# Optimization experiments

Hardware: AMD Instinct MI355X
Metric: run time of the kernel (lower is better)

The kernel has to match this reference:

```python
import jax, jax.numpy as jnp
import numpy as np

M, D, NI, L, NPL, R, T = 2, 128, 131072, 4, 2048, 8, 32
N = NI + L * NPL  # total DAG nodes


def setup_inputs() -> dict:
    key = jax.random.key(0)
    ks = jax.random.split(key, 18)
    thax = jax.random.randint(ks[0], (NI,), 0, T)
    sine = jax.random.uniform(ks[1], (NI,), jnp.float32)
    # parents of layer-l deriv nodes index any node built earlier (topological)
    raw = jax.random.randint(ks[2], (L, NPL, 2), 0, 2**30)
    bounds = jnp.array([NI + l * NPL for l in range(L)])[:, None, None]
    par = raw % bounds
    ridx = jax.random.randint(ks[3], (L, NPL), 0, R)
    pos = jax.random.uniform(ks[4], (N,), jnp.float32) + 0.01
    neg = jax.random.uniform(ks[5], (N,), jnp.float32) + 0.01
    s = 0.05
    return {
        'thax': thax, 'sine': sine, 'par': par, 'ridx': ridx,
        'pos': pos, 'neg': neg,
        'init_table': jax.random.normal(ks[6], (M, T, D)) * s,
        's_vec': jax.random.normal(ks[7], (M, D)) * s,
        'W1': jax.random.normal(ks[8], (M, R, 2 * D, D)) * s,
        'b1': jax.random.normal(ks[9], (M, R, D)) * s,
        'W2': jax.random.normal(ks[10], (M, R, D, D)) * s,
        'b2': jax.random.normal(ks[11], (M, R, D)) * s,
        'tweaks': jax.random.normal(ks[12], (M, 1, 2)) * s,
        'We1': jax.random.normal(ks[13], (M, D, D)) * s,
        'be1': jax.random.normal(ks[14], (M, D)) * s,
        'we2': jax.random.normal(ks[15], (M, D)) * s,
        'be2': jax.random.normal(ks[16], (M,)) * s,
    }


def reference(thax, sine, par, ridx, pos, neg, init_table, s_vec,
              W1, b1, W2, b2, tweaks, We1, be1, we2, be2):
    # init nodes: thax embedding + sine embellishment (per model)
    emb0 = init_table[:, thax, :] + sine[None, :, None] * s_vec[:, None, :]  # [M,NI,D]
    store = jnp.zeros((M, N, D), emb0.dtype).at[:, :NI].set(emb0)
    # topological layers of deriv nodes: gather parents, rule-indexed 2-layer MLP
    for l in range(L):
        p, r = par[l], ridx[l]
        cat = store[:, p].reshape(M, NPL, 2 * D)               # gather parents
        h = jax.nn.relu(jnp.einsum('mnc,mncd->mnd', cat, W1[:, r]) + b1[:, r])
        out = (jnp.einsum('mnd,mnde->mne', h, W2[:, r]) + b2[:, r]
               + tweaks[:, 0, 1][:, None, None])
        store = store.at[:, NI + l * NPL: NI + (l + 1) * NPL].set(out)
    # eval_net: per-node scalar logit (+ per-problem tweak)
    he = jax.nn.relu(jnp.einsum('mnd,mde->mne', store, We1) + be1[:, None, :])
    logit = jnp.einsum('mnd,md->mn', he, we2) + be2[:, None] + tweaks[:, 0, 0][:, None]
    tot_pos, tot_neg = pos.sum(), neg.sum()
    pw = tot_neg / tot_pos  # POS_WEIGHT_EXTRA = 1.0
    gold = pos / (pos + neg)
    w = pos + neg
    # BCEWithLogitsLoss(pos_weight=pw) per node, weighted by (pos+neg)
    bce = -(pw * gold[None] * jax.nn.log_sigmoid(logit)
            + (1.0 - gold[None]) * jax.nn.log_sigmoid(-logit))
    loss = (w[None] * bce).sum(axis=1)                          # [M]
    posOK = jnp.where(logit >= 0, pos[None], 0.0).sum(axis=1)
    negOK = jnp.where(logit < 0, neg[None], 0.0).sum(axis=1)
    return (loss, posOK, negOK, tot_pos, tot_neg)
```

## Files before the change

### kernel.cpp

```cpp
#include <hip/hip_runtime.h>
#include <hip/hip_bf16.h>

#define M_ 2
#define D_ 128
#define NI_ 131072
#define L_ 4
#define NPL_ 2048
#define R_ 8
#define T_ 32
#define N_ (NI_ + L_ * NPL_)
#define ND_ (L_ * NPL_)
#define PART3_ 1344

typedef __bf16 bf16x8 __attribute__((ext_vector_type(8)));
typedef float f32x4 __attribute__((ext_vector_type(4)));

#define OFF_W1T    0u
#define OFF_W2T    1048576u
#define OFF_WE1T   1572864u
#define OFF_TAB    1638400u
#define OFF_SVEC   1654784u
#define OFF_SORTED 1655296u
#define OFF_STARTS 1688064u
#define OFF_CNTF   1688192u
#define OFF_CNTA   1688320u
#define OFF_EA2    1688448u
#define OFF_EWB    1721216u
#define OFF_PA     1723264u
#define OFF_PB     1734016u
#define OFF_PPOK   1744768u
#define OFF_PNOK   1755520u
#define OFF_PTP    1766272u
#define OFF_PTN    1771648u
#define OFF_G      1777024u
#define OFF_STORE  2317696u
#define OFF_FSG    6512000u
#define OFF_CFG    6512032u
#define OFF_FLIST  6512064u

__device__ __forceinline__ unsigned short f2bu(float f) {
  unsigned int u = __float_as_uint(f);
  u += 0x7fffu + ((u >> 16) & 1u);
  return (unsigned short)(u >> 16);
}
__device__ __forceinline__ bf16x8 ldb8(const unsigned short* p) {
  return *reinterpret_cast<const bf16x8*>(p);
}

__device__ __forceinline__ bf16x8 node_chunk(int m, int row, int d0,
    const unsigned short* tab, const unsigned short* svec,
    const unsigned short* sd, const int* thax, const float* sine) {
  if (row < NI_) {
    bf16x8 tv = ldb8(&tab[(m * T_ + thax[row]) * D_ + d0]);
    bf16x8 sv = ldb8(&svec[m * D_ + d0]);
    float sn = sine[row];
    bf16x8 r;
#pragma unroll
    for (int j = 0; j < 8; ++j)
      r[j] = (__bf16)((float)tv[j] + sn * (float)sv[j]);
    return r;
  }
  return ldb8(&sd[(size_t)(m * ND_ + (row - NI_)) * D_ + d0]);
}

__global__ __launch_bounds__(256) void megaprep_kernel(
    const float* W1, const float* W2, const float* We1,
    const float* init_table, const float* s_vec,
    const float* b1, const float* be1, const float* we2,
    const int* ridx, const int* par,
    unsigned short* W1T, unsigned short* W2T, unsigned short* We1T,
    unsigned short* tab, unsigned short* svec,
    float* G, float* EA2, float* EWB,
    int* sorted, int* starts, int* cntF, int* cntA,
    int* fsg, int* cfg, int* fastlist, unsigned int* pzero) {
  __shared__ float smem[1056];
  __shared__ int icnt[16], ioff[16];
  int job = blockIdx.x;
  int tid = threadIdx.x;

  if (job < 800) {
    int z, rblk, cblk;
    if (job < 512)      { z = job >> 5;            rblk = (job & 31) >> 2; cblk = job & 3; }
    else if (job < 768) { int q = job - 512; z = 16 + (q >> 4); rblk = (q & 15) >> 2; cblk = q & 3; }
    else                { int q = job - 768; z = 32 + (q >> 4); rblk = (q & 15) >> 2; cblk = q & 3; }
    const float* src; unsigned short* dst; int R;
    if (z < 16)      { src = W1  + (size_t)z * 32768;        dst = W1T  + (size_t)z * 32768;        R = 256; }
    else if (z < 32) { src = W2  + (size_t)(z - 16) * 16384; dst = W2T  + (size_t)(z - 16) * 16384; R = 128; }
    else             { src = We1 + (size_t)(z - 32) * 16384; dst = We1T + (size_t)(z - 32) * 16384; R = 128; }
    int r0 = rblk * 32, c0 = cblk * 32;
    float (*tile)[33] = (float(*)[33])smem;
    int tx = tid & 31, ty = tid >> 5;
#pragma unroll
    for (int k = 0; k < 4; ++k)
      tile[ty + 8 * k][tx] = src[(size_t)(r0 + ty + 8 * k) * D_ + c0 + tx];
    __syncthreads();
#pragma unroll
    for (int k = 0; k < 4; ++k)
      dst[(size_t)(c0 + ty + 8 * k) * R + r0 + tx] = f2bu(tile[tx][ty + 8 * k]);
  } else if (job == 800) {
    for (int i = tid; i < 8448; i += 256) {
      if (i < 8192) tab[i] = f2bu(init_table[i]);
      else svec[i - 8192] = f2bu(s_vec[i - 8192]);
    }
  } else if (job < 1329) {
    int q = job - 801;
    int t = q / 16, mr = q & 15;
    int m = mr >> 3;
    int slot = tid >> 7, e = tid & 127;
    const float* vec = (t < 32) ? &init_table[(size_t)(m * T_ + t) * D_]
                                : &s_vec[(size_t)m * D_];
    if (tid < 128) smem[tid] = vec[tid];
    __syncthreads();
    const float* w = &W1[((size_t)mr * 256 + slot * 128) * D_];
    float acc = 0.f;
#pragma unroll 8
    for (int c = 0; c < 128; ++c) acc = fmaf(smem[c], w[c * D_ + e], acc);
    if (slot == 0 && t < 32) acc += b1[mr * D_ + e];
    G[((size_t)(mr * 2 + slot) * 33 + t) * D_ + e] = acc;
  } else if (job < 1363) {
    int q = job - 1329;
    int m = q / 17, t = (q % 17) * 2 + (tid >> 7);
    int e = tid & 127;
    if (t <= 32) {
      const float* vec = (t < 32) ? &init_table[(size_t)(m * T_ + t) * D_]
                                  : &s_vec[(size_t)m * D_];
      const float* w = &We1[(size_t)m * D_ * D_];
      float acc = 0.f;
#pragma unroll 8
      for (int d = 0; d < 128; ++d) acc = fmaf(vec[d], w[d * D_ + e], acc);
      if (t < 32) {
        EA2[m * 4096 + ((e >> 1) * 32 + t) * 2 + (e & 1)] = acc + be1[m * D_ + e];
      } else {
        EWB[(m * D_ + e) * 2 + 0] = acc;
        EWB[(m * D_ + e) * 2 + 1] = we2[m * D_ + e];
      }
    }
  } else if (job < 1367) {
    int l = job - 1363;
    if (tid < 16) icnt[tid] = 0;
    __syncthreads();
    for (int n = tid; n < NPL_; n += 256) {
      int r = ridx[l * NPL_ + n];
      int p0 = par[(l * NPL_ + n) * 2 + 0], p1 = par[(l * NPL_ + n) * 2 + 1];
      int slow = (p0 >= NI_ || p1 >= NI_) ? 1 : 0;
      atomicAdd(&icnt[r * 2 + slow], 1);
    }
    __syncthreads();
    if (tid == 0) {
      int run = 0;
      for (int b = 0; b < 16; ++b) { ioff[b] = run; run += icnt[b]; }
      for (int r = 0; r < R_; ++r) {
        starts[l * R_ + r] = ioff[2 * r];
        cntF[l * R_ + r] = icnt[2 * r];
        cntA[l * R_ + r] = icnt[2 * r] + icnt[2 * r + 1];
      }
    }
    __syncthreads();
    for (int n = tid; n < NPL_; n += 256) {
      int r = ridx[l * NPL_ + n];
      int p0 = par[(l * NPL_ + n) * 2 + 0], p1 = par[(l * NPL_ + n) * 2 + 1];
      int slow = (p0 >= NI_ || p1 >= NI_) ? 1 : 0;
      int p = atomicAdd(&ioff[r * 2 + slow], 1);
      sorted[l * NPL_ + p] = n;
    }
  } else if (job == 1367) {
    if (tid < 8) icnt[tid] = 0;
    __syncthreads();
    for (int g = tid; g < ND_; g += 256) {
      int p0 = par[2 * g], p1 = par[2 * g + 1];
      if (p0 < NI_ && p1 < NI_) atomicAdd(&icnt[ridx[g]], 1);
    }
    __syncthreads();
    if (tid == 0) {
      int run = 0;
      for (int r = 0; r < R_; ++r) {
        ioff[r] = run; fsg[r] = run; cfg[r] = icnt[r]; run += icnt[r];
      }
    }
    __syncthreads();
    for (int g = tid; g < ND_; g += 256) {
      int p0 = par[2 * g], p1 = par[2 * g + 1];
      if (p0 < NI_ && p1 < NI_) {
        int p = atomicAdd(&ioff[ridx[g]], 1);
        fastlist[p] = g;
      }
    }
  } else {
    for (int i = tid; i < 13440; i += 256) pzero[i] = 0u;
  }
}

__global__ __launch_bounds__(256) void main_kernel(
    const int* thax, const float* sine, const int* par,
    const float* pos, const float* neg,
    const float* b2, const float* tweaks,
    const float* G, const unsigned short* W2T, const unsigned short* We1T,
    const float* EA2, const float* EWB,
    const float* be1, const float* we2, const float* be2,
    const int* fsg, const int* cfg, const int* fastlist,
    unsigned short* sd,
    float* pA, float* pB, float* pPok, float* pNok, float* pTp, float* pTn) {
  __shared__ float sbuf[4448];
  int bid = blockIdx.x;
  int tid = threadIdx.x;
  int w = tid >> 6, lane = tid & 63;

  if (bid < 1280) {
    int m = bid / 640, q = bid % 640;
    int r = q / 80, tile = q % 80;
    int cnt = cfg[r];
    int base = tile * 16;
    if (base >= cnt) return;
    unsigned short* h_lds = (unsigned short*)sbuf;
    int*   t0a  = (int*)(sbuf + 1024);
    int*   t1a  = t0a + 16;
    float* s0a  = (float*)(t1a + 16);
    float* s1a  = s0a + 16;
    int*   gida = (int*)(s1a + 16);
    float* red2 = sbuf + 1104;
    if (tid < 16) {
      int loc = base + tid; if (loc >= cnt) loc = cnt - 1;
      int gid = fastlist[fsg[r] + loc];
      int p0 = par[2 * gid], p1 = par[2 * gid + 1];
      t0a[tid] = thax[p0]; s0a[tid] = sine[p0];
      t1a[tid] = thax[p1]; s1a[tid] = sine[p1];
      gida[tid] = gid;
    }
    __syncthreads();
    const float* Gm = &G[(size_t)(m * R_ + r) * 8448];
    {
      int row = tid >> 4, seg = tid & 15, d0 = seg * 8;
      int t0 = t0a[row], t1 = t1a[row];
      float s0 = s0a[row], s1 = s1a[row];
      const float* pa = &Gm[t0 * 128 + d0];
      const float* pb = &Gm[(33 + t1) * 128 + d0];
      const float* pu = &Gm[4096 + d0];
      const float* pv = &Gm[8320 + d0];
      bf16x8 hv;
#pragma unroll
      for (int half = 0; half < 2; ++half) {
        float4 a = *(const float4*)(pa + half * 4);
        float4 b = *(const float4*)(pb + half * 4);
        float4 u = *(const float4*)(pu + half * 4);
        float4 v = *(const float4*)(pv + half * 4);
        hv[half * 4 + 0] = (__bf16)fmaxf(a.x + b.x + s0 * u.x + s1 * v.x, 0.f);
        hv[half * 4 + 1] = (__bf16)fmaxf(a.y + b.y + s0 * u.y + s1 * v.y, 0.f);
        hv[half * 4 + 2] = (__bf16)fmaxf(a.z + b.z + s0 * u.z + s1 * v.z, 0.f);
        hv[half * 4 + 3] = (__bf16)fmaxf(a.w + b.w + s0 * u.w + s1 * v.w, 0.f);
      }
      *(bf16x8*)&h_lds[row * 128 + (d0 ^ ((row & 7) << 3))] = hv;
    }
    __syncthreads();
    int l15 = lane & 15, l4 = lane >> 4;
    const unsigned short* w2b = &W2T[(size_t)(m * R_ + r) * D_ * D_];
    f32x4 acc[2];
    acc[0] = (f32x4){0.f, 0.f, 0.f, 0.f};
    acc[1] = (f32x4){0.f, 0.f, 0.f, 0.f};
#pragma unroll
    for (int kc = 0; kc < 4; ++kc) {
      int d0 = kc * 32 + l4 * 8;
      bf16x8 a2 = ldb8(&h_lds[l15 * 128 + (d0 ^ ((l15 & 7) << 3))]);
#pragma unroll
      for (int f = 0; f < 2; ++f) {
        int fg = w * 2 + f;
        bf16x8 b = ldb8(&w2b[(fg * 16 + l15) * D_ + d0]);
        acc[f] = __builtin_amdgcn_mfma_f32_16x16x32_bf16(a2, b, acc[f], 0, 0, 0);
      }
    }
    float tw1 = tweaks[m * 2 + 1];
    const float* b2v = &b2[(m * R_ + r) * D_];
    __syncthreads();
#pragma unroll
    for (int i = 0; i < 4; ++i) {
      int row = l4 * 4 + i;
      int g = base + row;
#pragma unroll
      for (int f = 0; f < 2; ++f) {
        int e = (w * 2 + f) * 16 + l15;
        unsigned short val = f2bu(acc[f][i] + b2v[e] + tw1);
        h_lds[row * 128 + (e ^ ((row & 7) << 3))] = val;
        if (g < cnt) sd[(size_t)(m * ND_ + gida[row]) * D_ + e] = val;
      }
    }
    __syncthreads();
    f32x4 ae[2];
    ae[0] = (f32x4){0.f, 0.f, 0.f, 0.f};
    ae[1] = (f32x4){0.f, 0.f, 0.f, 0.f};
    const unsigned short* we1b = &We1T[(size_t)m * D_ * D_];
#pragma unroll
    for (int kc = 0; kc < 4; ++kc) {
      int d0 = kc * 32 + l4 * 8;
      bf16x8 a2 = ldb8(&h_lds[l15 * 128 + (d0 ^ ((l15 & 7) << 3))]);
#pragma unroll
      for (int f = 0; f < 2; ++f) {
        int fg = w * 2 + f;
        bf16x8 b = ldb8(&we1b[(fg * 16 + l15) * D_ + d0]);
        ae[f] = __builtin_amdgcn_mfma_f32_16x16x32_bf16(a2, b, ae[f], 0, 0, 0);
      }
    }
    float part[4] = {0.f, 0.f, 0.f, 0.f};
#pragma unroll
    for (int f = 0; f < 2; ++f) {
      int e = (w * 2 + f) * 16 + l15;
      float bb = be1[m * D_ + e];
      float wv = we2[m * D_ + e];
#pragma unroll
      for (int i = 0; i < 4; ++i) {
        float he = ae[f][i] + bb;
        he = he > 0.f ? he : 0.f;
        part[i] += he * wv;
      }
    }
#pragma unroll
    for (int mask = 1; mask < 16; mask <<= 1) {
#pragma unroll
      for (int i = 0; i < 4; ++i) part[i] += __shfl_xor(part[i], mask, 64);
    }
    if (l15 == 0) {
#pragma unroll
      for (int i = 0; i < 4; ++i) red2[w * 16 + l4 * 4 + i] = part[i];
    }
    __syncthreads();
    if (tid < 16) {
      int g = base + tid;
      float v6[6] = {0.f, 0.f, 0.f, 0.f, 0.f, 0.f};
      if (g < cnt) {
        float logit = red2[tid] + red2[16 + tid] + red2[32 + tid] + red2[48 + tid]
                    + be2[m] + tweaks[m * 2 + 0];
        int grow = NI_ + gida[tid];
        float p_ = pos[grow], n_ = neg[grow];
        float lse = log1pf(__expf(-fabsf(logit)));
        v6[0] = p_ * (fmaxf(-logit, 0.f) + lse);
        v6[1] = n_ * (fmaxf(logit, 0.f) + lse);
        v6[2] = logit >= 0.f ? p_ : 0.f;
        v6[3] = logit < 0.f ? n_ : 0.f;
        v6[4] = p_; v6[5] = n_;
      }
#pragma unroll
      for (int mask = 1; mask < 16; mask <<= 1) {
#pragma unroll
        for (int qq = 0; qq < 6; ++qq) v6[qq] += __shfl_xor(v6[qq], mask, 64);
      }
      if (tid == 0) {
        int slot = 512 + r * 80 + tile;
        pA[m * PART3_ + slot] = v6[0];
        pB[m * PART3_ + slot] = v6[1];
        pPok[m * PART3_ + slot] = v6[2];
        pNok[m * PART3_ + slot] = v6[3];
        if (m == 0) { pTp[slot] = v6[4]; pTn[slot] = v6[5]; }
      }
    }
  } else {
    int q = bid - 1280;
    int m = q >> 9, xb = q & 511;
    float* lea = sbuf;
    float* lwb = sbuf + 4096;
    float* red = sbuf + 4352;
    for (int i = tid; i < 4096; i += 256) lea[i] = EA2[m * 4096 + i];
    if (tid < 256) lwb[tid] = EWB[m * 256 + tid];
    __syncthreads();
    int row = xb * 256 + tid;
    int t = thax[row];
    float s = sine[row];
    float acc = 0.f;
#pragma unroll 8
    for (int p = 0; p < 64; ++p) {
      float2 ea = *(const float2*)&lea[(p * 32 + t) * 2];
      float4 wb = *(const float4*)&lwb[p * 4];
      float x0 = fmaf(s, wb.x, ea.x); x0 = fmaxf(x0, 0.f);
      acc = fmaf(x0, wb.y, acc);
      float x1 = fmaf(s, wb.z, ea.y); x1 = fmaxf(x1, 0.f);
      acc = fmaf(x1, wb.w, acc);
    }
    float logit = acc + be2[m] + tweaks[m * 2 + 0];
    float p_ = pos[row], n_ = neg[row];
    float lse = log1pf(__expf(-fabsf(logit)));
    float v[6];
    v[0] = p_ * (fmaxf(-logit, 0.f) + lse);
    v[1] = n_ * (fmaxf(logit, 0.f) + lse);
    v[2] = logit >= 0.f ? p_ : 0.f;
    v[3] = logit < 0.f ? n_ : 0.f;
    v[4] = p_; v[5] = n_;
#pragma unroll
    for (int mask = 1; mask < 64; mask <<= 1) {
#pragma unroll
      for (int k = 0; k < 6; ++k) v[k] += __shfl_xor(v[k], mask, 64);
    }
    if (lane == 0) {
#pragma unroll
      for (int k = 0; k < 6; ++k) red[k * 16 + w] = v[k];
    }
    __syncthreads();
    if (tid == 0) {
      float t6[6];
#pragma unroll
      for (int k = 0; k < 6; ++k)
        t6[k] = red[k * 16 + 0] + red[k * 16 + 1] + red[k * 16 + 2] + red[k * 16 + 3];
      pA[m * PART3_ + xb] = t6[0];
      pB[m * PART3_ + xb] = t6[1];
      pPok[m * PART3_ + xb] = t6[2];
      pNok[m * PART3_ + xb] = t6[3];
      if (m == 0) { pTp[xb] = t6[4]; pTn[xb] = t6[5]; }
    }
  }
}

__global__ __launch_bounds__(128) void slow_eval_kernel(int l,
    const int* thax, const float* sine, const int* par,
    const float* b1, const float* b2, const float* tweaks,
    const float* pos, const float* neg,
    const float* be1, const float* we2, const float* be2,
    const unsigned short* tab, const unsigned short* svec,
    const unsigned short* W1T, const unsigned short* W2T,
    const unsigned short* We1T,
    const int* sorted, const int* starts, const int* cntF, const int* cntA,
    unsigned short* sd,
    float* pA, float* pB, float* pPok, float* pNok, float* pTp, float* pTn) {
  int tile = blockIdx.x, r = blockIdx.y, m = blockIdx.z;
  int cF = cntF[l * R_ + r];
  int cS = cntA[l * R_ + r] - cF;
  int base = tile * 16;
  if (base >= cS) return;
  int start = starts[l * R_ + r] + cF;
  int tid = threadIdx.x;
  int w = tid >> 6, lane = tid & 63;
  int l15 = lane & 15, l4 = lane >> 4;
  __shared__ unsigned short h_lds[16 * 128];
  __shared__ float red2[32];

  int loc = base + l15; if (loc >= cS) loc = cS - 1;
  int node = sorted[l * NPL_ + start + loc];
  int p0 = par[(l * NPL_ + node) * 2 + 0];
  int p1 = par[(l * NPL_ + node) * 2 + 1];
  const unsigned short* w1b = &W1T[(size_t)(m * R_ + r) * D_ * 256];
  const unsigned short* w2b = &W2T[(size_t)(m * R_ + r) * D_ * D_];
  const unsigned short* we1b = &We1T[(size_t)m * D_ * D_];

  bf16x8 av[8];
#pragma unroll
  for (int kc = 0; kc < 8; ++kc) {
    int k = kc * 32 + l4 * 8;
    int p = (k < 128) ? p0 : p1;
    av[kc] = node_chunk(m, p, k & 127, tab, svec, sd, thax, sine);
  }
  f32x4 acch[4];
#pragma unroll
  for (int f = 0; f < 4; ++f) acch[f] = (f32x4){0.f, 0.f, 0.f, 0.f};
#pragma unroll
  for (int kc = 0; kc < 8; ++kc) {
    int k = kc * 32 + l4 * 8;
#pragma unroll
    for (int f = 0; f < 4; ++f) {
      int fg = w * 4 + f;
      bf16x8 b = ldb8(&w1b[(fg * 16 + l15) * 256 + k]);
      acch[f] = __builtin_amdgcn_mfma_f32_16x16x32_bf16(av[kc], b, acch[f], 0, 0, 0);
    }
  }
  const float* b1v = &b1[(m * R_ + r) * D_];
#pragma unroll
  for (int f = 0; f < 4; ++f) {
    int d = (w * 4 + f) * 16 + l15;
    float bb = b1v[d];
#pragma unroll
    for (int i = 0; i < 4; ++i) {
      int row = l4 * 4 + i;
      float h = acch[f][i] + bb;
      h = h > 0.f ? h : 0.f;
      h_lds[row * 128 + (d ^ ((row & 7) << 3))] = f2bu(h);
    }
  }
  __syncthreads();
  f32x4 acco[4];
#pragma unroll
  for (int f = 0; f < 4; ++f) acco[f] = (f32x4){0.f, 0.f, 0.f, 0.f};
#pragma unroll
  for (int kc = 0; kc < 4; ++kc) {
    int d0 = kc * 32 + l4 * 8;
    bf16x8 a2 = ldb8(&h_lds[l15 * 128 + (d0 ^ ((l15 & 7) << 3))]);
#pragma unroll
    for (int f = 0; f < 4; ++f) {
      int fg = w * 4 + f;
      bf16x8 b = ldb8(&w2b[(fg * 16 + l15) * D_ + d0]);
      acco[f] = __builtin_amdgcn_mfma_f32_16x16x32_bf16(a2, b, acco[f], 0, 0, 0);
    }
  }
  float tw1 = tweaks[m * 2 + 1];
  const float* b2v = &b2[(m * R_ + r) * D_];
  __syncthreads();
#pragma unroll
  for (int i = 0; i < 4; ++i) {
    int row = l4 * 4 + i;
    int g = base + row;
#pragma unroll
    for (int f = 0; f < 4; ++f) {
      int e = (w * 4 + f) * 16 + l15;
      unsigned short val = f2bu(acco[f][i] + b2v[e] + tw1);
      h_lds[row * 128 + (e ^ ((row & 7) << 3))] = val;
      if (g < cS) {
        int nd = sorted[l * NPL_ + start + g];
        sd[(size_t)(m * ND_ + l * NPL_ + nd) * D_ + e] = val;
      }
    }
  }
  __syncthreads();
  f32x4 ae[4];
#pragma unroll
  for (int f = 0; f < 4; ++f) ae[f] = (f32x4){0.f, 0.f, 0.f, 0.f};
#pragma unroll
  for (int kc = 0; kc < 4; ++kc) {
    int d0 = kc * 32 + l4 * 8;
    bf16x8 a2 = ldb8(&h_lds[l15 * 128 + (d0 ^ ((l15 & 7) << 3))]);
#pragma unroll
    for (int f = 0; f < 4; ++f) {
      int fg = w * 4 + f;
      bf16x8 b = ldb8(&we1b[(fg * 16 + l15) * D_ + d0]);
      ae[f] = __builtin_amdgcn_mfma_f32_16x16x32_bf16(a2, b, ae[f], 0, 0, 0);
    }
  }
  float part[4] = {0.f, 0.f, 0.f, 0.f};
#pragma unroll
  for (int f = 0; f < 4; ++f) {
    int e = (w * 4 + f) * 16 + l15;
    float bb = be1[m * D_ + e];
    float wv = we2[m * D_ + e];
#pragma unroll
    for (int i = 0; i < 4; ++i) {
      float he = ae[f][i] + bb;
      he = he > 0.f ? he : 0.f;
      part[i] += he * wv;
    }
  }
#pragma unroll
  for (int mask = 1; mask < 16; mask <<= 1) {
#pragma unroll
    for (int i = 0; i < 4; ++i) part[i] += __shfl_xor(part[i], mask, 64);
  }
  if (l15 == 0) {
#pragma unroll
    for (int i = 0; i < 4; ++i) red2[w * 16 + l4 * 4 + i] = part[i];
  }
  __syncthreads();
  if (tid < 16) {
    int g = base + tid;
    float v6[6] = {0.f, 0.f, 0.f, 0.f, 0.f, 0.f};
    if (g < cS) {
      float logit = red2[tid] + red2[16 + tid] + be2[m] + tweaks[m * 2 + 0];
      int nd = sorted[l * NPL_ + start + g];
      int grow = NI_ + l * NPL_ + nd;
      float p_ = pos[grow], n_ = neg[grow];
      float lse = log1pf(__expf(-fabsf(logit)));
      v6[0] = p_ * (fmaxf(-logit, 0.f) + lse);
      v6[1] = n_ * (fmaxf(logit, 0.f) + lse);
      v6[2] = logit >= 0.f ? p_ : 0.f;
      v6[3] = logit < 0.f ? n_ : 0.f;
      v6[4] = p_; v6[5] = n_;
    }
#pragma unroll
    for (int mask = 1; mask < 16; mask <<= 1) {
#pragma unroll
      for (int qq = 0; qq < 6; ++qq) v6[qq] += __shfl_xor(v6[qq], mask, 64);
    }
    if (tid == 0) {
      int slot = 1152 + (l - 1) * 64 + r * 8 + tile;
      pA[m * PART3_ + slot] = v6[0];
      pB[m * PART3_ + slot] = v6[1];
      pPok[m * PART3_ + slot] = v6[2];
      pNok[m * PART3_ + slot] = v6[3];
      if (m == 0) { pTp[slot] = v6[4]; pTn[slot] = v6[5]; }
    }
  }
}

__global__ __launch_bounds__(256) void finalize_kernel(
    const float* pA, const float* pB, const float* pPok, const float* pNok,
    const float* pTp, const float* pTn, float* out) {
  __shared__ float lred[10][4];
  const float* srcs[10] = {pA, pA + PART3_, pB, pB + PART3_,
                           pPok, pPok + PART3_, pNok, pNok + PART3_,
                           pTp, pTn};
  int tid = threadIdx.x;
  int w = tid >> 6, lane = tid & 63;
#pragma unroll
  for (int q = 0; q < 10; ++q) {
    float s = 0.f;
    for (int i = tid; i < PART3_; i += 256) s += srcs[q][i];
#pragma unroll
    for (int mask = 1; mask < 64; mask <<= 1) s += __shfl_xor(s, mask, 64);
    if (lane == 0) lred[q][w] = s;
  }
  __syncthreads();
  if (tid == 0) {
    float totals[10];
#pragma unroll
    for (int q = 0; q < 10; ++q)
      totals[q] = lred[q][0] + lred[q][1] + lred[q][2] + lred[q][3];
    float tp = totals[8], tn = totals[9];
    float pw = tn / tp;
    out[0] = pw * totals[0] + totals[2];
    out[1] = pw * totals[1] + totals[3];
    out[2] = totals[4]; out[3] = totals[5];
    out[4] = totals[6]; out[5] = totals[7];
    out[6] = tp; out[7] = tn;
  }
}

extern "C" void kernel_launch(void* const* d_in, const int* in_sizes, int n_in,
                              void* d_out, int out_size, void* d_ws, size_t ws_size,
                              hipStream_t stream) {
  const int*   thax = (const int*)d_in[0];
  const float* sine = (const float*)d_in[1];
  const int*   par  = (const int*)d_in[2];
  const int*   ridx = (const int*)d_in[3];
  const float* pos  = (const float*)d_in[4];
  const float* neg  = (const float*)d_in[5];
  const float* init_table = (const float*)d_in[6];
  const float* s_vec = (const float*)d_in[7];
  const float* W1 = (const float*)d_in[8];
  const float* b1 = (const float*)d_in[9];
  const float* W2 = (const float*)d_in[10];
  const float* b2 = (const float*)d_in[11];
  const float* tweaks = (const float*)d_in[12];
  const float* We1 = (const float*)d_in[13];
  const float* be1 = (const float*)d_in[14];
  const float* we2 = (const float*)d_in[15];
  const float* be2 = (const float*)d_in[16];

  char* ws = (char*)d_ws;
  unsigned short* W1T  = (unsigned short*)(ws + OFF_W1T);
  unsigned short* W2T  = (unsigned short*)(ws + OFF_W2T);
  unsigned short* We1T = (unsigned short*)(ws + OFF_WE1T);
  unsigned short* tab  = (unsigned short*)(ws + OFF_TAB);
  unsigned short* svec = (unsigned short*)(ws + OFF_SVEC);
  int* sorted = (int*)(ws + OFF_SORTED);
  int* starts = (int*)(ws + OFF_STARTS);
  int* cntF   = (int*)(ws + OFF_CNTF);
  int* cntA   = (int*)(ws + OFF_CNTA);
  float* EA2  = (float*)(ws + OFF_EA2);
  float* EWB  = (float*)(ws + OFF_EWB);
  float* pA   = (float*)(ws + OFF_PA);
  float* pB   = (float*)(ws + OFF_PB);
  float* pPok = (float*)(ws + OFF_PPOK);
  float* pNok = (float*)(ws + OFF_PNOK);
  float* pTp  = (float*)(ws + OFF_PTP);
  float* pTn  = (float*)(ws + OFF_PTN);
  float* G    = (float*)(ws + OFF_G);
  unsigned short* sd = (unsigned short*)(ws + OFF_STORE);
  int* fsg      = (int*)(ws + OFF_FSG);
  int* cfg      = (int*)(ws + OFF_CFG);
  int* fastlist = (int*)(ws + OFF_FLIST);

  megaprep_kernel<<<1369, 256, 0, stream>>>(
      W1, W2, We1, init_table, s_vec, b1, be1, we2, ridx, par,
      W1T, W2T, We1T, tab, svec, G, EA2, EWB, sorted, starts, cntF, cntA,
      fsg, cfg, fastlist, (unsigned int*)pA);
  main_kernel<<<2304, 256, 0, stream>>>(
      thax, sine, par, pos, neg, b2, tweaks, G, W2T, We1T, EA2, EWB,
      be1, we2, be2, fsg, cfg, fastlist, sd,
      pA, pB, pPok, pNok, pTp, pTn);
  for (int l = 1; l < L_; ++l) {
    slow_eval_kernel<<<dim3(8, R_, M_), 128, 0, stream>>>(
        l, thax, sine, par, b1, b2, tweaks, pos, neg, be1, we2, be2,
        tab, svec, W1T, W2T, We1T, sorted, starts, cntF, cntA, sd,
        pA, pB, pPok, pNok, pTp, pTn);
  }
  finalize_kernel<<<1, 256, 0, stream>>>(pA, pB, pPok, pNok, pTp, pTn,
                                         (float*)d_out);
}
```

Before: 100.7 us.

## Fold slow-node layers into main kernel via per-node ancestor recomputation

Drops the three per-layer slow_eval launches and the global derived-node store. Each slow (deep) node is now handled by its own block inside main_kernel, which walks its ancestor chain and recomputes the intermediate derived embeddings in shared memory with scalar FMAs. The prep kernel builds the fast and slow node lists with wave-ballot compaction and no longer transposes W1. This removes inter-layer launch serialization and store writes, at the cost of redundant recomputation, capped list capacities and scalar (non-MFMA) math for the slow nodes.

Result: faster. 92.43 us (-8.2%).

```diff
diff --git a/kernel.cpp b/kernel.cpp
--- a/kernel.cpp
+++ b/kernel.cpp
@@ -10,57 +10,43 @@
 #define T_ 32
 #define N_ (NI_ + L_ * NPL_)
 #define ND_ (L_ * NPL_)
-#define PART3_ 1344
+#define PSTRIDE_ 1792
+#define PUSED_ 1665
+#define FCAP_ 1280
+#define SCAP_ 512
+#define CCAP_ 24
 
 typedef __bf16 bf16x8 __attribute__((ext_vector_type(8)));
 typedef float f32x4 __attribute__((ext_vector_type(4)));
-
-#define OFF_W1T    0u
-#define OFF_W2T    1048576u
-#define OFF_WE1T   1572864u
-#define OFF_TAB    1638400u
-#define OFF_SVEC   1654784u
-#define OFF_SORTED 1655296u
-#define OFF_STARTS 1688064u
-#define OFF_CNTF   1688192u
-#define OFF_CNTA   1688320u
-#define OFF_EA2    1688448u
-#define OFF_EWB    1721216u
-#define OFF_PA     1723264u
-#define OFF_PB     1734016u
-#define OFF_PPOK   1744768u
-#define OFF_PNOK   1755520u
-#define OFF_PTP    1766272u
-#define OFF_PTN    1771648u
-#define OFF_G      1777024u
-#define OFF_STORE  2317696u
-#define OFF_FSG    6512000u
-#define OFF_CFG    6512032u
-#define OFF_FLIST  6512064u
+typedef unsigned short u16x4 __attribute__((ext_vector_type(4)));
+
+#define OFF_W2T    0u
+#define OFF_WE1T   524288u
+#define OFF_TAB    589824u
+#define OFF_SVEC   606208u
+#define OFF_EA2    606720u
+#define OFF_EWB    639488u
+#define OFF_PA     641536u
+#define OFF_PB     655872u
+#define OFF_PPOK   670208u
+#define OFF_PNOK   684544u
+#define OFF_PTP    698880u
+#define OFF_PTN    706048u
+#define OFF_G      713216u
+#define OFF_FLIST  1253888u
+#define OFF_SLIST  1294848u
+#define OFF_CFG    1296896u
 
 __device__ __forceinline__ unsigned short f2bu(float f) {
   unsigned int u = __float_as_uint(f);
   u += 0x7fffu + ((u >> 16) & 1u);
   return (unsigned short)(u >> 16);
 }
+__device__ __forceinline__ float bfu2f(unsigned short u) {
+  return __uint_as_float((unsigned int)u << 16);
+}
 __device__ __forceinline__ bf16x8 ldb8(const unsigned short* p) {
   return *reinterpret_cast<const bf16x8*>(p);
-}
-
-__device__ __forceinline__ bf16x8 node_chunk(int m, int row, int d0,
-    const unsigned short* tab, const unsigned short* svec,
-    const unsigned short* sd, const int* thax, const float* sine) {
-  if (row < NI_) {
-    bf16x8 tv = ldb8(&tab[(m * T_ + thax[row]) * D_ + d0]);
-    bf16x8 sv = ldb8(&svec[m * D_ + d0]);
-    float sn = sine[row];
-    bf16x8 r;
-#pragma unroll
-    for (int j = 0; j < 8; ++j)
-      r[j] = (__bf16)((float)tv[j] + sn * (float)sv[j]);
-    return r;
-  }
-  return ldb8(&sd[(size_t)(m * ND_ + (row - NI_)) * D_ + d0]);
 }
 
 __global__ __launch_bounds__(256) void megaprep_kernel(
@@ -68,57 +54,54 @@
     const float* init_table, const float* s_vec,
     const float* b1, const float* be1, const float* we2,
     const int* ridx, const int* par,
-    unsigned short* W1T, unsigned short* W2T, unsigned short* We1T,
+    unsigned short* W2T, unsigned short* We1T,
     unsigned short* tab, unsigned short* svec,
     float* G, float* EA2, float* EWB,
-    int* sorted, int* starts, int* cntF, int* cntA,
-    int* fsg, int* cfg, int* fastlist, unsigned int* pzero) {
+    int* fastlist, int* slowlist, int* cfg, unsigned int* pzero) {
   __shared__ float smem[1056];
-  __shared__ int icnt[16], ioff[16];
+  __shared__ int lcnt;
   int job = blockIdx.x;
   int tid = threadIdx.x;
 
-  if (job < 800) {
-    int z, rblk, cblk;
-    if (job < 512)      { z = job >> 5;            rblk = (job & 31) >> 2; cblk = job & 3; }
-    else if (job < 768) { int q = job - 512; z = 16 + (q >> 4); rblk = (q & 15) >> 2; cblk = q & 3; }
-    else                { int q = job - 768; z = 32 + (q >> 4); rblk = (q & 15) >> 2; cblk = q & 3; }
-    const float* src; unsigned short* dst; int R;
-    if (z < 16)      { src = W1  + (size_t)z * 32768;        dst = W1T  + (size_t)z * 32768;        R = 256; }
-    else if (z < 32) { src = W2  + (size_t)(z - 16) * 16384; dst = W2T  + (size_t)(z - 16) * 16384; R = 128; }
-    else             { src = We1 + (size_t)(z - 32) * 16384; dst = We1T + (size_t)(z - 32) * 16384; R = 128; }
-    int r0 = rblk * 32, c0 = cblk * 32;
-    float (*tile)[33] = (float(*)[33])smem;
-    int tx = tid & 31, ty = tid >> 5;
-#pragma unroll
-    for (int k = 0; k < 4; ++k)
-      tile[ty + 8 * k][tx] = src[(size_t)(r0 + ty + 8 * k) * D_ + c0 + tx];
-    __syncthreads();
-#pragma unroll
-    for (int k = 0; k < 4; ++k)
-      dst[(size_t)(c0 + ty + 8 * k) * R + r0 + tx] = f2bu(tile[tx][ty + 8 * k]);
-  } else if (job == 800) {
+  if (job < 9) {
+    int* out; int cap;
+    if (job < 8) { out = fastlist + job * FCAP_; cap = FCAP_; }
+    else         { out = slowlist;               cap = SCAP_; }
+    if (tid == 0) lcnt = 0;
+    __syncthreads();
+    int lane = tid & 63;
+    unsigned long long lmask_lt = (1ull << lane) - 1ull;
+    for (int g = tid; g < ND_; g += 256) {
+      int p0 = par[2 * g], p1 = par[2 * g + 1];
+      bool fast = (p0 < NI_) && (p1 < NI_);
+      bool match = (job < 8) ? (fast && ridx[g] == job) : (!fast);
+      unsigned long long mask = __ballot(match);
+      if (mask) {
+        int leader = __ffsll((unsigned long long)mask) - 1;
+        int pre = __popcll(mask & lmask_lt);
+        int base_ = 0;
+        if (lane == leader) base_ = atomicAdd(&lcnt, __popcll(mask));
+        base_ = __shfl(base_, leader, 64);
+        if (match) {
+          int idx = base_ + pre;
+          if (idx < cap) out[idx] = g;
+        }
+      }
+    }
+    __syncthreads();
+    if (tid == 0) {
+      int c = lcnt; if (c > cap) c = cap;
+      cfg[job] = c;
+    }
+  } else if (job == 9) {
+    for (int i = tid; i < 17920; i += 256) pzero[i] = 0u;
+  } else if (job == 10) {
     for (int i = tid; i < 8448; i += 256) {
       if (i < 8192) tab[i] = f2bu(init_table[i]);
       else svec[i - 8192] = f2bu(s_vec[i - 8192]);
     }
-  } else if (job < 1329) {
-    int q = job - 801;
-    int t = q / 16, mr = q & 15;
-    int m = mr >> 3;
-    int slot = tid >> 7, e = tid & 127;
-    const float* vec = (t < 32) ? &init_table[(size_t)(m * T_ + t) * D_]
-                                : &s_vec[(size_t)m * D_];
-    if (tid < 128) smem[tid] = vec[tid];
-    __syncthreads();
-    const float* w = &W1[((size_t)mr * 256 + slot * 128) * D_];
-    float acc = 0.f;
-#pragma unroll 8
-    for (int c = 0; c < 128; ++c) acc = fmaf(smem[c], w[c * D_ + e], acc);
-    if (slot == 0 && t < 32) acc += b1[mr * D_ + e];
-    G[((size_t)(mr * 2 + slot) * 33 + t) * D_ + e] = acc;
-  } else if (job < 1363) {
-    int q = job - 1329;
+  } else if (job < 45) {
+    int q = job - 11;
     int m = q / 17, t = (q % 17) * 2 + (tid >> 7);
     int e = tid & 127;
     if (t <= 32) {
@@ -135,70 +118,56 @@
         EWB[(m * D_ + e) * 2 + 1] = we2[m * D_ + e];
       }
     }
-  } else if (job < 1367) {
-    int l = job - 1363;
-    if (tid < 16) icnt[tid] = 0;
-    __syncthreads();
-    for (int n = tid; n < NPL_; n += 256) {
-      int r = ridx[l * NPL_ + n];
-      int p0 = par[(l * NPL_ + n) * 2 + 0], p1 = par[(l * NPL_ + n) * 2 + 1];
-      int slow = (p0 >= NI_ || p1 >= NI_) ? 1 : 0;
-      atomicAdd(&icnt[r * 2 + slow], 1);
-    }
-    __syncthreads();
-    if (tid == 0) {
-      int run = 0;
-      for (int b = 0; b < 16; ++b) { ioff[b] = run; run += icnt[b]; }
-      for (int r = 0; r < R_; ++r) {
-        starts[l * R_ + r] = ioff[2 * r];
-        cntF[l * R_ + r] = icnt[2 * r];
-        cntA[l * R_ + r] = icnt[2 * r] + icnt[2 * r + 1];
-      }
-    }
-    __syncthreads();
-    for (int n = tid; n < NPL_; n += 256) {
-      int r = ridx[l * NPL_ + n];
-      int p0 = par[(l * NPL_ + n) * 2 + 0], p1 = par[(l * NPL_ + n) * 2 + 1];
-      int slow = (p0 >= NI_ || p1 >= NI_) ? 1 : 0;
-      int p = atomicAdd(&ioff[r * 2 + slow], 1);
-      sorted[l * NPL_ + p] = n;
-    }
-  } else if (job == 1367) {
-    if (tid < 8) icnt[tid] = 0;
-    __syncthreads();
-    for (int g = tid; g < ND_; g += 256) {
-      int p0 = par[2 * g], p1 = par[2 * g + 1];
-      if (p0 < NI_ && p1 < NI_) atomicAdd(&icnt[ridx[g]], 1);
-    }
-    __syncthreads();
-    if (tid == 0) {
-      int run = 0;
-      for (int r = 0; r < R_; ++r) {
-        ioff[r] = run; fsg[r] = run; cfg[r] = icnt[r]; run += icnt[r];
-      }
-    }
-    __syncthreads();
-    for (int g = tid; g < ND_; g += 256) {
-      int p0 = par[2 * g], p1 = par[2 * g + 1];
-      if (p0 < NI_ && p1 < NI_) {
-        int p = atomicAdd(&ioff[ridx[g]], 1);
-        fastlist[p] = g;
-      }
-    }
+  } else if (job < 573) {
+    int q = job - 45;
+    int t = q / 16, mr = q & 15;
+    int m = mr >> 3;
+    int slot = tid >> 7, e = tid & 127;
+    const float* vec = (t < 32) ? &init_table[(size_t)(m * T_ + t) * D_]
+                                : &s_vec[(size_t)m * D_];
+    if (tid < 128) smem[tid] = vec[tid];
+    __syncthreads();
+    const float* w = &W1[((size_t)mr * 256 + slot * 128) * D_];
+    float acc = 0.f;
+#pragma unroll 8
+    for (int c = 0; c < 128; ++c) acc = fmaf(smem[c], w[c * D_ + e], acc);
+    if (slot == 0 && t < 32) acc += b1[mr * D_ + e];
+    G[((size_t)(mr * 2 + slot) * 33 + t) * D_ + e] = acc;
   } else {
-    for (int i = tid; i < 13440; i += 256) pzero[i] = 0u;
+    int q0 = job - 573;
+    const float* src; unsigned short* dst;
+    int rblk, cblk;
+    if (q0 < 256) {
+      int z = q0 >> 4;
+      src = W2 + (size_t)z * 16384; dst = W2T + (size_t)z * 16384;
+      rblk = (q0 & 15) >> 2; cblk = q0 & 3;
+    } else {
+      int q = q0 - 256; int z = q >> 4;
+      src = We1 + (size_t)z * 16384; dst = We1T + (size_t)z * 16384;
+      rblk = (q & 15) >> 2; cblk = q & 3;
+    }
+    int r0 = rblk * 32, c0 = cblk * 32;
+    float (*tile)[33] = (float(*)[33])smem;
+    int tx = tid & 31, ty = tid >> 5;
+#pragma unroll
+    for (int k = 0; k < 4; ++k)
+      tile[ty + 8 * k][tx] = src[(size_t)(r0 + ty + 8 * k) * D_ + c0 + tx];
+    __syncthreads();
+#pragma unroll
+    for (int k = 0; k < 4; ++k)
+      dst[(size_t)(c0 + ty + 8 * k) * D_ + r0 + tx] = f2bu(tile[tx][ty + 8 * k]);
   }
 }
 
 __global__ __launch_bounds__(256) void main_kernel(
-    const int* thax, const float* sine, const int* par,
+    const int* thax, const float* sine, const int* par, const int* ridx,
     const float* pos, const float* neg,
-    const float* b2, const float* tweaks,
+    const float* W1, const float* b1, const float* b2, const float* tweaks,
     const float* G, const unsigned short* W2T, const unsigned short* We1T,
+    const unsigned short* tab, const unsigned short* svec,
     const float* EA2, const float* EWB,
     const float* be1, const float* we2, const float* be2,
-    const int* fsg, const int* cfg, const int* fastlist,
-    unsigned short* sd,
+    const int* cfg, const int* fastlist, const int* slowlist,
     float* pA, float* pB, float* pPok, float* pNok, float* pTp, float* pTn) {
   __shared__ float sbuf[4448];
   int bid = blockIdx.x;
@@ -220,7 +189,7 @@
     float* red2 = sbuf + 1104;
     if (tid < 16) {
       int loc = base + tid; if (loc >= cnt) loc = cnt - 1;
-      int gid = fastlist[fsg[r] + loc];
+      int gid = fastlist[r * FCAP_ + loc];
       int p0 = par[2 * gid], p1 = par[2 * gid + 1];
       t0a[tid] = thax[p0]; s0a[tid] = sine[p0];
       t1a[tid] = thax[p1]; s1a[tid] = sine[p1];
@@ -273,13 +242,10 @@
 #pragma unroll
     for (int i = 0; i < 4; ++i) {
       int row = l4 * 4 + i;
-      int g = base + row;
 #pragma unroll
       for (int f = 0; f < 2; ++f) {
         int e = (w * 2 + f) * 16 + l15;
-        unsigned short val = f2bu(acc[f][i] + b2v[e] + tw1);
-        h_lds[row * 128 + (e ^ ((row & 7) << 3))] = val;
-        if (g < cnt) sd[(size_t)(m * ND_ + gida[row]) * D_ + e] = val;
+        h_lds[row * 128 + (e ^ ((row & 7) << 3))] = f2bu(acc[f][i] + b2v[e] + tw1);
       }
     }
     __syncthreads();
@@ -323,7 +289,7 @@
     __syncthreads();
     if (tid < 16) {
       int g = base + tid;
-      float v6[6] = {0.f, 0.f, 0.f, 0.f, 0.f, 0.f};
+      float v6[4] = {0.f, 0.f, 0.f, 0.f};
       if (g < cnt) {
         float logit = red2[tid] + red2[16 + tid] + red2[32 + tid] + red2[48 + tid]
                     + be2[m] + tweaks[m * 2 + 0];
@@ -334,23 +300,21 @@
         v6[1] = n_ * (fmaxf(logit, 0.f) + lse);
         v6[2] = logit >= 0.f ? p_ : 0.f;
         v6[3] = logit < 0.f ? n_ : 0.f;
-        v6[4] = p_; v6[5] = n_;
       }
 #pragma unroll
       for (int mask = 1; mask < 16; mask <<= 1) {
 #pragma unroll
-        for (int qq = 0; qq < 6; ++qq) v6[qq] += __shfl_xor(v6[qq], mask, 64);
+        for (int qq = 0; qq < 4; ++qq) v6[qq] += __shfl_xor(v6[qq], mask, 64);
       }
       if (tid == 0) {
         int slot = 512 + r * 80 + tile;
-        pA[m * PART3_ + slot] = v6[0];
-        pB[m * PART3_ + slot] = v6[1];
-        pPok[m * PART3_ + slot] = v6[2];
-        pNok[m * PART3_ + slot] = v6[3];
-        if (m == 0) { pTp[slot] = v6[4]; pTn[slot] = v6[5]; }
-      }
-    }
-  } else {
+        pA[m * PSTRIDE_ + slot] = v6[0];
+        pB[m * PSTRIDE_ + slot] = v6[1];
+        pPok[m * PSTRIDE_ + slot] = v6[2];
+        pNok[m * PSTRIDE_ + slot] = v6[3];
+      }
+    }
+  } else if (bid < 2304) {
     int q = bid - 1280;
     int m = q >> 9, xb = q & 511;
     float* lea = sbuf;
@@ -396,177 +360,174 @@
 #pragma unroll
       for (int k = 0; k < 6; ++k)
         t6[k] = red[k * 16 + 0] + red[k * 16 + 1] + red[k * 16 + 2] + red[k * 16 + 3];
-      pA[m * PART3_ + xb] = t6[0];
-      pB[m * PART3_ + xb] = t6[1];
-      pPok[m * PART3_ + xb] = t6[2];
-      pNok[m * PART3_ + xb] = t6[3];
+      pA[m * PSTRIDE_ + xb] = t6[0];
+      pB[m * PSTRIDE_ + xb] = t6[1];
+      pPok[m * PSTRIDE_ + xb] = t6[2];
+      pNok[m * PSTRIDE_ + xb] = t6[3];
       if (m == 0) { pTp[xb] = t6[4]; pTn[xb] = t6[5]; }
     }
-  }
-}
-
-__global__ __launch_bounds__(128) void slow_eval_kernel(int l,
-    const int* thax, const float* sine, const int* par,
-    const float* b1, const float* b2, const float* tweaks,
-    const float* pos, const float* neg,
-    const float* be1, const float* we2, const float* be2,
-    const unsigned short* tab, const unsigned short* svec,
-    const unsigned short* W1T, const unsigned short* W2T,
-    const unsigned short* We1T,
-    const int* sorted, const int* starts, const int* cntF, const int* cntA,
-    unsigned short* sd,
-    float* pA, float* pB, float* pPok, float* pNok, float* pTp, float* pTn) {
-  int tile = blockIdx.x, r = blockIdx.y, m = blockIdx.z;
-  int cF = cntF[l * R_ + r];
-  int cS = cntA[l * R_ + r] - cF;
-  int base = tile * 16;
-  if (base >= cS) return;
-  int start = starts[l * R_ + r] + cF;
-  int tid = threadIdx.x;
-  int w = tid >> 6, lane = tid & 63;
-  int l15 = lane & 15, l4 = lane >> 4;
-  __shared__ unsigned short h_lds[16 * 128];
-  __shared__ float red2[32];
-
-  int loc = base + l15; if (loc >= cS) loc = cS - 1;
-  int node = sorted[l * NPL_ + start + loc];
-  int p0 = par[(l * NPL_ + node) * 2 + 0];
-  int p1 = par[(l * NPL_ + node) * 2 + 1];
-  const unsigned short* w1b = &W1T[(size_t)(m * R_ + r) * D_ * 256];
-  const unsigned short* w2b = &W2T[(size_t)(m * R_ + r) * D_ * D_];
-  const unsigned short* we1b = &We1T[(size_t)m * D_ * D_];
-
-  bf16x8 av[8];
-#pragma unroll
-  for (int kc = 0; kc < 8; ++kc) {
-    int k = kc * 32 + l4 * 8;
-    int p = (k < 128) ? p0 : p1;
-    av[kc] = node_chunk(m, p, k & 127, tab, svec, sd, thax, sine);
-  }
-  f32x4 acch[4];
-#pragma unroll
-  for (int f = 0; f < 4; ++f) acch[f] = (f32x4){0.f, 0.f, 0.f, 0.f};
-#pragma unroll
-  for (int kc = 0; kc < 8; ++kc) {
-    int k = kc * 32 + l4 * 8;
-#pragma unroll
-    for (int f = 0; f < 4; ++f) {
-      int fg = w * 4 + f;
-      bf16x8 b = ldb8(&w1b[(fg * 16 + l15) * 256 + k]);
-      acch[f] = __builtin_amdgcn_mfma_f32_16x16x32_bf16(av[kc], b, acch[f], 0, 0, 0);
-    }
-  }
-  const float* b1v = &b1[(m * R_ + r) * D_];
-#pragma unroll
-  for (int f = 0; f < 4; ++f) {
-    int d = (w * 4 + f) * 16 + l15;
-    float bb = b1v[d];
-#pragma unroll
-    for (int i = 0; i < 4; ++i) {
-      int row = l4 * 4 + i;
-      float h = acch[f][i] + bb;
-      h = h > 0.f ? h : 0.f;
-      h_lds[row * 128 + (d ^ ((row & 7) << 3))] = f2bu(h);
-    }
-  }
-  __syncthreads();
-  f32x4 acco[4];
-#pragma unroll
-  for (int f = 0; f < 4; ++f) acco[f] = (f32x4){0.f, 0.f, 0.f, 0.f};
-#pragma unroll
-  for (int kc = 0; kc < 4; ++kc) {
-    int d0 = kc * 32 + l4 * 8;
-    bf16x8 a2 = ldb8(&h_lds[l15 * 128 + (d0 ^ ((l15 & 7) << 3))]);
-#pragma unroll
-    for (int f = 0; f < 4; ++f) {
-      int fg = w * 4 + f;
-      bf16x8 b = ldb8(&w2b[(fg * 16 + l15) * D_ + d0]);
-      acco[f] = __builtin_amdgcn_mfma_f32_16x16x32_bf16(a2, b, acco[f], 0, 0, 0);
-    }
-  }
-  float tw1 = tweaks[m * 2 + 1];
-  const float* b2v = &b2[(m * R_ + r) * D_];
-  __syncthreads();
-#pragma unroll
-  for (int i = 0; i < 4; ++i) {
-    int row = l4 * 4 + i;
-    int g = base + row;
-#pragma unroll
-    for (int f = 0; f < 4; ++f) {
-      int e = (w * 4 + f) * 16 + l15;
-      unsigned short val = f2bu(acco[f][i] + b2v[e] + tw1);
-      h_lds[row * 128 + (e ^ ((row & 7) << 3))] = val;
-      if (g < cS) {
-        int nd = sorted[l * NPL_ + start + g];
-        sd[(size_t)(m * ND_ + l * NPL_ + nd) * D_ + e] = val;
-      }
-    }
-  }
-  __syncthreads();
-  f32x4 ae[4];
-#pragma unroll
-  for (int f = 0; f < 4; ++f) ae[f] = (f32x4){0.f, 0.f, 0.f, 0.f};
-#pragma unroll
-  for (int kc = 0; kc < 4; ++kc) {
-    int d0 = kc * 32 + l4 * 8;
-    bf16x8 a2 = ldb8(&h_lds[l15 * 128 + (d0 ^ ((l15 & 7) << 3))]);
-#pragma unroll
-    for (int f = 0; f < 4; ++f) {
-      int fg = w * 4 + f;
-      bf16x8 b = ldb8(&we1b[(fg * 16 + l15) * D_ + d0]);
-      ae[f] = __builtin_amdgcn_mfma_f32_16x16x32_bf16(a2, b, ae[f], 0, 0, 0);
-    }
-  }
-  float part[4] = {0.f, 0.f, 0.f, 0.f};
-#pragma unroll
-  for (int f = 0; f < 4; ++f) {
-    int e = (w * 4 + f) * 16 + l15;
-    float bb = be1[m * D_ + e];
-    float wv = we2[m * D_ + e];
-#pragma unroll
-    for (int i = 0; i < 4; ++i) {
-      float he = ae[f][i] + bb;
+  } else if (bid < 2306) {
+    int j = bid - 2304;
+    float* red = sbuf;
+    const float* src = j ? neg : pos;
+    float s = 0.f;
+    for (int i = NI_ + tid; i < N_; i += 256) s += src[i];
+#pragma unroll
+    for (int mask = 1; mask < 64; mask <<= 1) s += __shfl_xor(s, mask, 64);
+    if (lane == 0) red[w] = s;
+    __syncthreads();
+    if (tid == 0) {
+      float t = red[0] + red[1] + red[2] + red[3];
+      if (j == 0) pTp[1152] = t; else pTn[1152] = t;
+    }
+  } else {
+    int q = bid - 2306;
+    int m = q >> 9, si = q & 511;
+    if (si >= cfg[8]) return;
+    int*   list  = (int*)sbuf;
+    int*   meta  = (int*)(sbuf + 24);
+    unsigned short* catl = (unsigned short*)(sbuf + 32);
+    float* hbuf  = sbuf + 160;
+    float* hp0   = sbuf + 288;
+    float* hp1   = sbuf + 416;
+    unsigned short* cache = (unsigned short*)(sbuf + 544);
+
+    int g_row = slowlist[si];
+    if (tid == 0) {
+      int nn = 0;
+      list[nn++] = g_row;
+      for (int i = 0; i < nn; ++i) {
+        int g = list[i];
+        for (int s = 0; s < 2; ++s) {
+          int p = par[2 * g + s];
+          if (p >= NI_) {
+            int pg = p - NI_;
+            bool found = false;
+            for (int jj = 0; jj < nn; ++jj) if (list[jj] == pg) { found = true; break; }
+            if (!found && nn < CCAP_) list[nn++] = pg;
+          }
+        }
+      }
+      for (int i = 1; i < nn; ++i) {
+        int v = list[i]; int jj = i - 1;
+        while (jj >= 0 && list[jj] > v) { list[jj + 1] = list[jj]; --jj; }
+        list[jj + 1] = v;
+      }
+      meta[0] = nn;
+    }
+    __syncthreads();
+    int NN = meta[0];
+    float tw1 = tweaks[m * 2 + 1];
+    for (int j = 0; j < NN; ++j) {
+      int g = list[j];
+      int r = ridx[g];
+      int p0 = par[2 * g], p1 = par[2 * g + 1];
+      bool fastn = (p0 < NI_) && (p1 < NI_);
+      if (fastn) {
+        if (tid < 128) {
+          int d = tid;
+          const float* Gm = &G[(size_t)(m * R_ + r) * 8448];
+          float hv = Gm[thax[p0] * 128 + d] + Gm[(33 + thax[p1]) * 128 + d]
+                   + sine[p0] * Gm[4096 + d] + sine[p1] * Gm[8320 + d];
+          hbuf[d] = bfu2f(f2bu(fmaxf(hv, 0.f)));
+        }
+        __syncthreads();
+      } else {
+        if (tid == 0) {
+          int s0 = -1, s1 = -1;
+          if (p0 >= NI_) for (int jj = 0; jj < j; ++jj) if (list[jj] == p0 - NI_) { s0 = jj; break; }
+          if (p1 >= NI_) for (int jj = 0; jj < j; ++jj) if (list[jj] == p1 - NI_) { s1 = jj; break; }
+          meta[1] = s0; meta[2] = s1;
+        }
+        __syncthreads();
+        {
+          int c = tid; int p = (c < 128) ? p0 : p1; int cc = c & 127;
+          int slot = (c < 128) ? meta[1] : meta[2];
+          unsigned short v;
+          if (p < NI_) {
+            float tv = bfu2f(tab[(m * T_ + thax[p]) * D_ + cc])
+                     + sine[p] * bfu2f(svec[m * D_ + cc]);
+            v = f2bu(tv);
+          } else {
+            v = cache[slot * 128 + cc];
+          }
+          catl[c] = v;
+        }
+        __syncthreads();
+        int d = tid & 127, half = tid >> 7;
+        const float* w1r = &W1[(((size_t)(m * R_ + r)) * 256 + half * 128) * D_];
+        float acc = 0.f;
+#pragma unroll 8
+        for (int c = 0; c < 128; ++c)
+          acc = fmaf(bfu2f(catl[half * 128 + c]), w1r[(size_t)c * D_ + d], acc);
+        if (half == 0) hp0[d] = acc; else hp1[d] = acc;
+        __syncthreads();
+        if (tid < 128) {
+          float hv = b1[(m * R_ + r) * D_ + tid] + hp0[tid] + hp1[tid];
+          hbuf[tid] = bfu2f(f2bu(fmaxf(hv, 0.f)));
+        }
+        __syncthreads();
+      }
+      {
+        int e = tid & 127, half = tid >> 7;
+        const u16x4* w2r4 = (const u16x4*)&W2T[((size_t)(m * R_ + r) * D_ + e) * D_ + half * 64];
+        float acc = 0.f;
+#pragma unroll
+        for (int dd = 0; dd < 16; ++dd) {
+          u16x4 wv = w2r4[dd];
+          int db = half * 64 + dd * 4;
+          acc = fmaf(bfu2f(wv[0]), hbuf[db + 0], acc);
+          acc = fmaf(bfu2f(wv[1]), hbuf[db + 1], acc);
+          acc = fmaf(bfu2f(wv[2]), hbuf[db + 2], acc);
+          acc = fmaf(bfu2f(wv[3]), hbuf[db + 3], acc);
+        }
+        if (half == 0) hp0[e] = acc; else hp1[e] = acc;
+      }
+      __syncthreads();
+      if (tid < 128) {
+        float o = hp0[tid] + hp1[tid] + b2[(m * R_ + r) * D_ + tid] + tw1;
+        cache[j * 128 + tid] = f2bu(o);
+      }
+      __syncthreads();
+    }
+    int jr = NN - 1;
+    {
+      int e = tid & 127, half = tid >> 7;
+      const u16x4* wer4 = (const u16x4*)&We1T[((size_t)m * D_ + e) * D_ + half * 64];
+      float acc = 0.f;
+#pragma unroll
+      for (int dd = 0; dd < 16; ++dd) {
+        u16x4 wv = wer4[dd];
+        int db = half * 64 + dd * 4;
+        acc = fmaf(bfu2f(wv[0]), bfu2f(cache[jr * 128 + db + 0]), acc);
+        acc = fmaf(bfu2f(wv[1]), bfu2f(cache[jr * 128 + db + 1]), acc);
+        acc = fmaf(bfu2f(wv[2]), bfu2f(cache[jr * 128 + db + 2]), acc);
+        acc = fmaf(bfu2f(wv[3]), bfu2f(cache[jr * 128 + db + 3]), acc);
+      }
+      if (half == 0) hp0[e] = acc; else hp1[e] = acc;
+    }
+    __syncthreads();
+    if (tid < 128) {
+      float he = hp0[tid] + hp1[tid] + be1[m * D_ + tid];
       he = he > 0.f ? he : 0.f;
-      part[i] += he * wv;
-    }
-  }
-#pragma unroll
-  for (int mask = 1; mask < 16; mask <<= 1) {
-#pragma unroll
-    for (int i = 0; i < 4; ++i) part[i] += __shfl_xor(part[i], mask, 64);
-  }
-  if (l15 == 0) {
-#pragma unroll
-    for (int i = 0; i < 4; ++i) red2[w * 16 + l4 * 4 + i] = part[i];
-  }
-  __syncthreads();
-  if (tid < 16) {
-    int g = base + tid;
-    float v6[6] = {0.f, 0.f, 0.f, 0.f, 0.f, 0.f};
-    if (g < cS) {
-      float logit = red2[tid] + red2[16 + tid] + be2[m] + tweaks[m * 2 + 0];
-      int nd = sorted[l * NPL_ + start + g];
-      int grow = NI_ + l * NPL_ + nd;
-      float p_ = pos[grow], n_ = neg[grow];
-      float lse = log1pf(__expf(-fabsf(logit)));
-      v6[0] = p_ * (fmaxf(-logit, 0.f) + lse);
-      v6[1] = n_ * (fmaxf(logit, 0.f) + lse);
-      v6[2] = logit >= 0.f ? p_ : 0.f;
-      v6[3] = logit < 0.f ? n_ : 0.f;
-      v6[4] = p_; v6[5] = n_;
-    }
-#pragma unroll
-    for (int mask = 1; mask < 16; mask <<= 1) {
-#pragma unroll
-      for (int qq = 0; qq < 6; ++qq) v6[qq] += __shfl_xor(v6[qq], mask, 64);
-    }
-    if (tid == 0) {
-      int slot = 1152 + (l - 1) * 64 + r * 8 + tile;
-      pA[m * PART3_ + slot] = v6[0];
-      pB[m * PART3_ + slot] = v6[1];
-      pPok[m * PART3_ + slot] = v6[2];
-      pNok[m * PART3_ + slot] = v6[3];
-      if (m == 0) { pTp[slot] = v6[4]; pTn[slot] = v6[5]; }
+      hbuf[tid] = he * we2[m * D_ + tid];
+    }
+    __syncthreads();
+    if (tid < 64) {
+      float s = hbuf[tid] + hbuf[tid + 64];
+#pragma unroll
+      for (int mask = 1; mask < 64; mask <<= 1) s += __shfl_xor(s, mask, 64);
+      if (tid == 0) {
+        float logit = s + be2[m] + tweaks[m * 2 + 0];
+        int grow = NI_ + g_row;
+        float p_ = pos[grow], n_ = neg[grow];
+        float lse = log1pf(__expf(-fabsf(logit)));
+        int slot = 1153 + si;
+        pA[m * PSTRIDE_ + slot] = p_ * (fmaxf(-logit, 0.f) + lse);
+        pB[m * PSTRIDE_ + slot] = n_ * (fmaxf(logit, 0.f) + lse);
+        pPok[m * PSTRIDE_ + slot] = logit >= 0.f ? p_ : 0.f;
+        pNok[m * PSTRIDE_ + slot] = logit < 0.f ? n_ : 0.f;
+      }
     }
   }
 }
@@ -575,15 +536,15 @@
     const float* pA, const float* pB, const float* pPok, const float* pNok,
     const float* pTp, const float* pTn, float* out) {
   __shared__ float lred[10][4];
-  const float* srcs[10] = {pA, pA + PART3_, pB, pB + PART3_,
-                           pPok, pPok + PART3_, pNok, pNok + PART3_,
+  const float* srcs[10] = {pA, pA + PSTRIDE_, pB, pB + PSTRIDE_,
+                           pPok, pPok + PSTRIDE_, pNok, pNok + PSTRIDE_,
                            pTp, pTn};
   int tid = threadIdx.x;
   int w = tid >> 6, lane = tid & 63;
 #pragma unroll
   for (int q = 0; q < 10; ++q) {
     float s = 0.f;
-    for (int i = tid; i < PART3_; i += 256) s += srcs[q][i];
+    for (int i = tid; i < PUSED_; i += 256) s += srcs[q][i];
 #pragma unroll
     for (int mask = 1; mask < 64; mask <<= 1) s += __shfl_xor(s, mask, 64);
     if (lane == 0) lred[q][w] = s;
@@ -626,15 +587,10 @@
   const float* be2 = (const float*)d_in[16];
 
   char* ws = (char*)d_ws;
-  unsigned short* W1T  = (unsigned short*)(ws + OFF_W1T);
   unsigned short* W2T  = (unsigned short*)(ws + OFF_W2T);
   unsigned short* We1T = (unsigned short*)(ws + OFF_WE1T);
   unsigned short* tab  = (unsigned short*)(ws + OFF_TAB);
   unsigned short* svec = (unsigned short*)(ws + OFF_SVEC);
-  int* sorted = (int*)(ws + OFF_SORTED);
-  int* starts = (int*)(ws + OFF_STARTS);
-  int* cntF   = (int*)(ws + OFF_CNTF);
-  int* cntA   = (int*)(ws + OFF_CNTA);
   float* EA2  = (float*)(ws + OFF_EA2);
   float* EWB  = (float*)(ws + OFF_EWB);
   float* pA   = (float*)(ws + OFF_PA);
@@ -644,25 +600,19 @@
   float* pTp  = (float*)(ws + OFF_PTP);
   float* pTn  = (float*)(ws + OFF_PTN);
   float* G    = (float*)(ws + OFF_G);
-  unsigned short* sd = (unsigned short*)(ws + OFF_STORE);
-  int* fsg      = (int*)(ws + OFF_FSG);
+  int* fastlist = (int*)(ws + OFF_FLIST);
+  int* slowlist = (int*)(ws + OFF_SLIST);
   int* cfg      = (int*)(ws + OFF_CFG);
-  int* fastlist = (int*)(ws + OFF_FLIST);
-
-  megaprep_kernel<<<1369, 256, 0, stream>>>(
+
+  megaprep_kernel<<<861, 256, 0, stream>>>(
       W1, W2, We1, init_table, s_vec, b1, be1, we2, ridx, par,
-      W1T, W2T, We1T, tab, svec, G, EA2, EWB, sorted, starts, cntF, cntA,
-      fsg, cfg, fastlist, (unsigned int*)pA);
-  main_kernel<<<2304, 256, 0, stream>>>(
-      thax, sine, par, pos, neg, b2, tweaks, G, W2T, We1T, EA2, EWB,
-      be1, we2, be2, fsg, cfg, fastlist, sd,
+      W2T, We1T, tab, svec, G, EA2, EWB,
+      fastlist, slowlist, cfg, (unsigned int*)pA);
+  main_kernel<<<3330, 256, 0, stream>>>(
+      thax, sine, par, ridx, pos, neg, W1, b1, b2, tweaks,
+      G, W2T, We1T, tab, svec, EA2, EWB, be1, we2, be2,
+      cfg, fastlist, slowlist,
       pA, pB, pPok, pNok, pTp, pTn);
-  for (int l = 1; l < L_; ++l) {
-    slow_eval_kernel<<<dim3(8, R_, M_), 128, 0, stream>>>(
-        l, thax, sine, par, b1, b2, tweaks, pos, neg, be1, we2, be2,
-        tab, svec, W1T, W2T, We1T, sorted, starts, cntF, cntA, sd,
-        pA, pB, pPok, pNok, pTp, pTn);
-  }
   finalize_kernel<<<1, 256, 0, stream>>>(pA, pB, pPok, pNok, pTp, pTn,
                                          (float*)d_out);
 }
```
